# Kernel tuning notes

Hardware: AMD Instinct MI355X
Metric: run time of the kernel (lower is better)

## Reference

```python
import jax, jax.numpy as jnp
import numpy as np

N_QUBITS = 20
EVO_SUPPORT = (2, 5)
CHAIN_QUBIT = 0


def _apply_operator(state, op, support):
    """Apply batched operator op (2^k, 2^k, B) to state (2,)*n + (B,) on `support` qubits.

    Faithful to pyqtorch's apply_operator: reshape op to (2,)*2k + (B,) and contract
    the support axes, keeping the batch axis aligned.
    """
    n = state.ndim - 1
    k = len(support)
    B = state.shape[-1]
    op = op.reshape((2,) * (2 * k) + (B,))
    letters = 'abcdefghijklmnopqrstuvwxyz'
    s_l = list(letters[:n])          # state qubit axes
    b = letters[n]                   # batch axis
    out_l = list(letters[n + 1:n + 1 + k])
    in_l = [s_l[q] for q in support]
    op_str = ''.join(out_l) + ''.join(in_l) + b
    st_str = ''.join(s_l) + b
    res = list(s_l)
    for q, o in zip(support, out_l):
        res[q] = o
    return jnp.einsum(f"{op_str},{st_str}->{''.join(res) + b}", op, state)


def setup_inputs() -> dict:
    key = jax.random.key(0)
    ks = jax.random.split(key, 6)
    B = 16
    dim = 2 ** N_QUBITS
    return {
        'state_re': jax.random.normal(ks[0], (dim, B), jnp.float32),
        'state_im': jax.random.normal(ks[1], (dim, B), jnp.float32),
        'hmat_re': jax.random.normal(ks[2], (4, 4, B), jnp.float32),
        'hmat_im': jax.random.normal(ks[3], (4, 4, B), jnp.float32),
        'theta': jax.random.uniform(ks[4], (8, B), jnp.float32),
        'tvals': jax.random.uniform(ks[5], (B,), jnp.float32),
    }


def reference(state_re, state_im, hmat_re, hmat_im, theta, tvals):
    n = N_QUBITS
    B = state_re.shape[-1]
    state = (state_re + 1j * state_im).astype(jnp.complex64).reshape((2,) * n + (B,))

    # --- PyQComposedBlock: chain of single-qubit RX gates composed via reduce(bmm, reversed) ---
    half = 0.5 * theta                      # (N_ops, B)
    c = jnp.cos(half).astype(jnp.complex64)
    s = jnp.sin(half).astype(jnp.complex64)
    # U_k: [[c, -i s], [-i s, c]] per op, batch-first layout (N_ops, B, 2, 2)
    U = jnp.stack([jnp.stack([c, -1j * s], axis=-1),
                   jnp.stack([-1j * s, c], axis=-1)], axis=-2)
    acc = U[-1]
    for i in range(U.shape[0] - 2, -1, -1):  # reduce(bmm, reversed(ops)): U_{N-1} @ ... @ U_0
        acc = acc @ U[i]
    state = _apply_operator(state, jnp.moveaxis(acc, 0, -1), (CHAIN_QUBIT,))

    # --- PyQHamiltonianEvolution: U = exp(-i t H) on a 2-qubit support ---
    A = (hmat_re + 1j * hmat_im).astype(jnp.complex64)       # (4, 4, B)
    H = 0.5 * (A + jnp.conj(jnp.swapaxes(A, 0, 1)))          # Hermitian generator
    Hb = jnp.moveaxis(H, -1, 0)                              # (B, 4, 4)
    evals, V = jnp.linalg.eigh(Hb)                           # H Hermitian -> exact matrix exp
    phase = jnp.exp(-1j * tvals[:, None] * evals)            # (B, 4)
    Ue = jnp.einsum('bij,bj,bkj->bik', V, phase.astype(jnp.complex64), jnp.conj(V))
    state = _apply_operator(state, jnp.moveaxis(Ue, 0, -1), EVO_SUPPORT)

    # --- Observable: total magnetization sum_q Z_q (AddPyQOperation of diagonal Z ops) ---
    w = jnp.zeros((2,) * n, jnp.float32)
    z = jnp.array([1.0, -1.0], jnp.float32)
    for q in range(n):
        w = w + z.reshape((1,) * q + (2,) + (1,) * (n - 1 - q))
    opsi = state * w[..., None]
    # expectation Re<psi|O|psi> per batch element
    return jnp.real(jnp.sum(jnp.conj(state) * opsi, axis=tuple(range(n))))
```

## Files before the change

### kernel.cpp

```cpp
#include <hip/hip_runtime.h>
#include <math.h>

constexpr int NQ     = 20;
constexpr int DIM    = 1 << NQ;
constexpr int B      = 16;
constexpr int GROUPS = 1 << 17;
constexpr int GPB    = 32;
constexpr int TILES  = GROUPS / GPB;
constexpr int NBLK   = 1024;
constexpr int TPB    = TILES / NBLK;
constexpr int NTHR   = 512;


__global__ __launch_bounds__(256) void prep_kernel(
    const float* __restrict__ hre, const float* __restrict__ him,
    const float* __restrict__ theta, const float* __restrict__ tv,
    float* __restrict__ ws) {
  __shared__ double Mre[16][16], Mim[16][16];
  __shared__ double Are[16][16], Aim[16][16];
  __shared__ double Bre[16][16], Bim[16][16];
  __shared__ double nrm[16][4];
  __shared__ int    scl[16];
  __shared__ int    scmax_s;

  int t = threadIdx.x;
  int b = t >> 4, e = t & 15, i = e >> 2, j = e & 3;

  if (t == 0) scmax_s = 0;

  if (e == 0) {
    double th = 0.0;
    for (int k = 0; k < 8; k++) th += (double)theta[k * B + b];
    th *= 0.5;
    ws[b]     = (float)cos(th);
    ws[B + b] = (float)sin(th);
  }

  {
    double tt  = (double)tv[b];
    double are = hre[(i*4+j)*B + b], aim = him[(i*4+j)*B + b];
    double cre = hre[(j*4+i)*B + b], cim = him[(j*4+i)*B + b];
    double Hre = 0.5*(are + cre), Him = 0.5*(aim - cim);
    Mre[b][e] = tt * Him;
    Mim[b][e] = -tt * Hre;
  }
  __syncthreads();

  if (j == 0) {
    double r = 0.0;
    for (int m = 0; m < 4; m++) r += fabs(Mre[b][i*4+m]) + fabs(Mim[b][i*4+m]);
    nrm[b][i] = r;
  }
  __syncthreads();
  if (e == 0) {
    double ninf = fmax(fmax(nrm[b][0], nrm[b][1]), fmax(nrm[b][2], nrm[b][3]));
    int sc = 0;
    while (ninf > 0.25 && sc < 40) { ninf *= 0.5; sc++; }
    scl[b] = sc;
    atomicMax(&scmax_s, sc);
  }
  __syncthreads();
  int sc = scl[b];
  int scmax = scmax_s;
  {
    double scale = ldexp(1.0, -sc);
    Mre[b][e] *= scale; Mim[b][e] *= scale;
  }
  Are[b][e] = (i == j) ? 1.0 : 0.0;
  Aim[b][e] = 0.0;
  __syncthreads();

  double (*Tr)[16] = Are; double (*Ti)[16] = Aim;
  double (*Pr)[16] = Bre; double (*Pi)[16] = Bim;

  for (int k = 13; k >= 1; k--) {
    double rr = 0.0, ii = 0.0;
    for (int m = 0; m < 4; m++) {
      double mr = Mre[b][i*4+m], mi = Mim[b][i*4+m];
      double xr = Tr[b][m*4+j],  xi = Ti[b][m*4+j];
      rr += mr*xr - mi*xi;
      ii += mr*xi + mi*xr;
    }
    double inv = 1.0 / (double)k;
    Pr[b][e] = rr*inv + ((i == j) ? 1.0 : 0.0);
    Pi[b][e] = ii*inv;
    { double (*s)[16] = Tr; Tr = Pr; Pr = s; s = Ti; Ti = Pi; Pi = s; }
    __syncthreads();
  }
  for (int q = 0; q < scmax; q++) {
    double rr, ii;
    if (q < sc) {
      rr = 0.0; ii = 0.0;
      for (int m = 0; m < 4; m++) {
        double xr = Tr[b][i*4+m], xi = Ti[b][i*4+m];
        double yr = Tr[b][m*4+j], yi = Ti[b][m*4+j];
        rr += xr*yr - xi*yi;
        ii += xr*yi + xi*yr;
      }
    } else { rr = Tr[b][e]; ii = Ti[b][e]; }
    Pr[b][e] = rr; Pi[b][e] = ii;
    { double (*s)[16] = Tr; Tr = Pr; Pr = s; s = Ti; Ti = Pi; Pi = s; }
    __syncthreads();
  }

  float* ue = ws + 2*B + b*32;
  ue[e*2]     = (float)Tr[b][e];
  ue[e*2 + 1] = (float)Ti[b][e];
}

__global__ __launch_bounds__(NTHR, 6) void fused_kernel(
    const float* __restrict__ sre, const float* __restrict__ sim,
    const float* __restrict__ ws, float* __restrict__ partial) {
  __shared__ float st[16 * 512];
  __shared__ float red[16];

  int t = threadIdx.x;
  if (t < 16) red[t] = 0.f;

  int b  = t & 15;
  int gl = t >> 4;
  float c = ws[b], s = ws[B + b];
  float ur[4][4], ui[4][4];
  {
    const float* ue = ws + 2 * B + b * 32;
    #pragma unroll
    for (int i = 0; i < 4; i++) {
      float4 p0 = *(const float4*)(ue + i * 8);
      float4 p1 = *(const float4*)(ue + i * 8 + 4);
      ur[i][0] = p0.x; ui[i][0] = p0.y; ur[i][1] = p0.z; ui[i][1] = p0.w;
      ur[i][2] = p1.x; ui[i][2] = p1.y; ur[i][3] = p1.z; ui[i][3] = p1.w;
    }
  }

  int l  = t & 63;
  int wv = t >> 6;
  float acc = 0.f;

  for (int tt = 0; tt < TPB; tt++) {
    int g0 = (blockIdx.x * TPB + tt) * GPB;
    int base0 = (g0 & 0x3FFF) | ((g0 & 0xC000) << 1) | ((g0 & 0x10000) << 2);

    #pragma unroll
    for (int p = 0; p < 4; p++) {
      int cb    = p * 512 + wv * 64;
      int panel = cb >> 7;
      int wofs  = (cb & 127) << 2;
      int j     = panel >> 1;
      const float* src = (panel & 1) ? sim : sre;
      int off = (((j >> 2) & 1) << 19) | (((j >> 1) & 1) << 17) | ((j & 1) << 14);
      const float* gsrc = src + (size_t)(base0 + off) * 16 + wofs + l * 4;
      float* ldst = &st[panel * 512 + wofs];
      __builtin_amdgcn_global_load_lds(
          (const __attribute__((address_space(1))) void*)gsrc,
          (__attribute__((address_space(3))) void*)ldst,
          16, 0, 0);
    }
    __syncthreads();

    float ar[8], ai[8];
    #pragma unroll
    for (int j = 0; j < 8; j++) {
      ar[j] = st[(2 * j) * 512 + t];
      ai[j] = st[(2 * j + 1) * 512 + t];
    }

    #pragma unroll
    for (int j = 0; j < 4; j++) {
      float xr = ar[j], xi = ai[j], yr = ar[j+4], yi = ai[j+4];
      ar[j]   = c*xr + s*yi;   ai[j]   = c*xi - s*yr;
      ar[j+4] = s*xi + c*yr;   ai[j+4] = c*yi - s*xr;
    }

    int base = base0 + gl;
    int pc = __popc(base);
    float wb = (float)(17 - 2*pc);
    #pragma unroll
    for (int h = 0; h < 2; h++) {
      float w0 = wb + (h ? -1.f : 1.f);
      #pragma unroll
      for (int k = 0; k < 4; k++) {
        float rr = 0.f, ii = 0.f;
        #pragma unroll
        for (int m = 0; m < 4; m++) {
          float xr = ar[h*4+m], xi = ai[h*4+m];
          rr = fmaf(ur[k][m], xr, rr); rr = fmaf(-ui[k][m], xi, rr);
          ii = fmaf(ur[k][m], xi, ii); ii = fmaf(ui[k][m], xr, ii);
        }
        int sb = ((k>>1)&1) + (k&1);
        float w = w0 + (float)(2 - 2*sb);
        acc = fmaf(rr*rr + ii*ii, w, acc);
      }
    }
    __syncthreads();
  }

  acc += __shfl_xor(acc, 16, 64);
  acc += __shfl_xor(acc, 32, 64);

  if ((t & 63) < 16) atomicAdd(&red[t & 15], acc);
  __syncthreads();
  if (t < 16) partial[blockIdx.x * 16 + t] = red[t];
}

__global__ void reduce_kernel(const float* __restrict__ partial, float* __restrict__ out) {
  int t = threadIdx.x;
  int b = t & 15;
  float acc = 0.f;
  for (int i = t >> 4; i < NBLK; i += 16)
    acc += partial[i * 16 + b];
  acc += __shfl_xor(acc, 16, 64);
  acc += __shfl_xor(acc, 32, 64);
  __shared__ float red[16];
  if (t < 16) red[t] = 0.f;
  __syncthreads();
  if ((t & 63) < 16) atomicAdd(&red[t & 15], acc);
  __syncthreads();
  if (t < 16) out[t] = red[t];
}

extern "C" void kernel_launch(void* const* d_in, const int* in_sizes, int n_in,
                              void* d_out, int out_size, void* d_ws, size_t ws_size,
                              hipStream_t stream) {
  const float* sre = (const float*)d_in[0];
  const float* sim = (const float*)d_in[1];
  const float* hre = (const float*)d_in[2];
  const float* him = (const float*)d_in[3];
  const float* th  = (const float*)d_in[4];
  const float* tv  = (const float*)d_in[5];

  float* ws = (float*)d_ws;
  float* partial = ws + 544;

  prep_kernel<<<1, 256, 0, stream>>>(hre, him, th, tv, ws);
  fused_kernel<<<NBLK, NTHR, 0, stream>>>(sre, sim, ws, partial);
  reduce_kernel<<<1, 256, 0, stream>>>(partial, (float*)d_out);
}
```

Before: 177.7 us.

## Fuse prep, main and reduce kernels into one launch with last-block reduction

Every block now recomputes the small matrix exponential and RX rotation itself in shared memory, reusing the state-tile LDS pool, so the separate prep kernel goes away. The final reduction is done by whichever block finishes last, detected through a global atomic counter, so the separate reduce kernel also goes away. This removes two launches and their serial dependencies. In exchange each block repeats the serial double-precision prep work with many syncthreads, adds a memset, and lowers the launch-bounds occupancy hint from 6 to 2.

After: 424.4 us. +138.8%, slower.

```diff
diff --git a/kernel.cpp b/kernel.cpp
--- a/kernel.cpp
+++ b/kernel.cpp
@@ -11,124 +11,131 @@
 constexpr int TPB    = TILES / NBLK;
 constexpr int NTHR   = 512;
 
-
-__global__ __launch_bounds__(256) void prep_kernel(
+__global__ __launch_bounds__(NTHR, 2) void mega_kernel(
+    const float* __restrict__ sre, const float* __restrict__ sim,
     const float* __restrict__ hre, const float* __restrict__ him,
     const float* __restrict__ theta, const float* __restrict__ tv,
-    float* __restrict__ ws) {
-  __shared__ double Mre[16][16], Mim[16][16];
-  __shared__ double Are[16][16], Aim[16][16];
-  __shared__ double Bre[16][16], Bim[16][16];
+    float* __restrict__ partial, unsigned* __restrict__ cnt,
+    float* __restrict__ out) {
+  __shared__ double pool[4096];
+  __shared__ __align__(16) float u_f[16 * 36];
+  __shared__ float cs_lds[32];
+  __shared__ float red[16];
   __shared__ double nrm[16][4];
   __shared__ int    scl[16];
   __shared__ int    scmax_s;
+  __shared__ int    lastflag;
+
+  float*  st  = (float*)pool;
+  double* Mre = pool;
+  double* Mim = pool + 256;
+  double* Ar  = pool + 512;
+  double* Ai  = pool + 768;
+  double* Br  = pool + 1024;
+  double* Bi  = pool + 1280;
 
   int t = threadIdx.x;
-  int b = t >> 4, e = t & 15, i = e >> 2, j = e & 3;
-
-  if (t == 0) scmax_s = 0;
-
-  if (e == 0) {
-    double th = 0.0;
-    for (int k = 0; k < 8; k++) th += (double)theta[k * B + b];
-    th *= 0.5;
-    ws[b]     = (float)cos(th);
-    ws[B + b] = (float)sin(th);
-  }
+  if (t == 0) { scmax_s = 0; lastflag = 0; }
+  if (t < 16) red[t] = 0.f;
+  __syncthreads();
 
   {
-    double tt  = (double)tv[b];
-    double are = hre[(i*4+j)*B + b], aim = him[(i*4+j)*B + b];
-    double cre = hre[(j*4+i)*B + b], cim = him[(j*4+i)*B + b];
-    double Hre = 0.5*(are + cre), Him = 0.5*(aim - cim);
-    Mre[b][e] = tt * Him;
-    Mim[b][e] = -tt * Hre;
-  }
-  __syncthreads();
-
-  if (j == 0) {
-    double r = 0.0;
-    for (int m = 0; m < 4; m++) r += fabs(Mre[b][i*4+m]) + fabs(Mim[b][i*4+m]);
-    nrm[b][i] = r;
-  }
-  __syncthreads();
-  if (e == 0) {
-    double ninf = fmax(fmax(nrm[b][0], nrm[b][1]), fmax(nrm[b][2], nrm[b][3]));
-    int sc = 0;
-    while (ninf > 0.25 && sc < 40) { ninf *= 0.5; sc++; }
-    scl[b] = sc;
-    atomicMax(&scmax_s, sc);
-  }
-  __syncthreads();
-  int sc = scl[b];
-  int scmax = scmax_s;
-  {
-    double scale = ldexp(1.0, -sc);
-    Mre[b][e] *= scale; Mim[b][e] *= scale;
-  }
-  Are[b][e] = (i == j) ? 1.0 : 0.0;
-  Aim[b][e] = 0.0;
-  __syncthreads();
-
-  double (*Tr)[16] = Are; double (*Ti)[16] = Aim;
-  double (*Pr)[16] = Bre; double (*Pi)[16] = Bim;
-
-  for (int k = 13; k >= 1; k--) {
-    double rr = 0.0, ii = 0.0;
-    for (int m = 0; m < 4; m++) {
-      double mr = Mre[b][i*4+m], mi = Mim[b][i*4+m];
-      double xr = Tr[b][m*4+j],  xi = Ti[b][m*4+j];
-      rr += mr*xr - mi*xi;
-      ii += mr*xi + mi*xr;
-    }
-    double inv = 1.0 / (double)k;
-    Pr[b][e] = rr*inv + ((i == j) ? 1.0 : 0.0);
-    Pi[b][e] = ii*inv;
-    { double (*s)[16] = Tr; Tr = Pr; Pr = s; s = Ti; Ti = Pi; Pi = s; }
-    __syncthreads();
-  }
-  for (int q = 0; q < scmax; q++) {
-    double rr, ii;
-    if (q < sc) {
-      rr = 0.0; ii = 0.0;
-      for (int m = 0; m < 4; m++) {
-        double xr = Tr[b][i*4+m], xi = Ti[b][i*4+m];
-        double yr = Tr[b][m*4+j], yi = Ti[b][m*4+j];
-        rr += xr*yr - xi*yi;
-        ii += xr*yi + xi*yr;
+    int pb = (t >> 4) & 15, e = t & 15, i = e >> 2, j = e & 3;
+    bool act = (t < 256);
+
+    if (act && e == 0) {
+      double th = 0.0;
+      for (int k = 0; k < 8; k++) th += (double)theta[k * B + pb];
+      th *= 0.5;
+      cs_lds[pb]      = (float)cos(th);
+      cs_lds[16 + pb] = (float)sin(th);
+    }
+    if (act) {
+      double tt  = (double)tv[pb];
+      double are = hre[(i*4+j)*B + pb], aim = him[(i*4+j)*B + pb];
+      double cre = hre[(j*4+i)*B + pb], cim = him[(j*4+i)*B + pb];
+      double Hre = 0.5*(are + cre), Him = 0.5*(aim - cim);
+      Mre[pb*16 + e] = tt * Him;
+      Mim[pb*16 + e] = -tt * Hre;
+    }
+    __syncthreads();
+    if (act && j == 0) {
+      double r = 0.0;
+      for (int m = 0; m < 4; m++) r += fabs(Mre[pb*16 + i*4+m]) + fabs(Mim[pb*16 + i*4+m]);
+      nrm[pb][i] = r;
+    }
+    __syncthreads();
+    if (act && e == 0) {
+      double ninf = fmax(fmax(nrm[pb][0], nrm[pb][1]), fmax(nrm[pb][2], nrm[pb][3]));
+      int sc = 0;
+      while (ninf > 0.25 && sc < 40) { ninf *= 0.5; sc++; }
+      scl[pb] = sc;
+      atomicMax(&scmax_s, sc);
+    }
+    __syncthreads();
+    int scmax = scmax_s;
+    int sc = act ? scl[pb] : 0;
+    if (act) {
+      double scale = ldexp(1.0, -sc);
+      Mre[pb*16+e] *= scale; Mim[pb*16+e] *= scale;
+      Ar[pb*16+e] = (i == j) ? 1.0 : 0.0;
+      Ai[pb*16+e] = 0.0;
+    }
+    __syncthreads();
+
+    double *Tr = Ar, *Ti = Ai, *Pr = Br, *Pi = Bi;
+    for (int k = 13; k >= 1; k--) {
+      if (act) {
+        double rr = 0.0, ii = 0.0;
+        for (int m = 0; m < 4; m++) {
+          double mr = Mre[pb*16 + i*4+m], mi = Mim[pb*16 + i*4+m];
+          double xr = Tr[pb*16 + m*4+j], xi = Ti[pb*16 + m*4+j];
+          rr += mr*xr - mi*xi;
+          ii += mr*xi + mi*xr;
+        }
+        double inv = 1.0 / (double)k;
+        Pr[pb*16+e] = rr*inv + ((i == j) ? 1.0 : 0.0);
+        Pi[pb*16+e] = ii*inv;
       }
-    } else { rr = Tr[b][e]; ii = Ti[b][e]; }
-    Pr[b][e] = rr; Pi[b][e] = ii;
-    { double (*s)[16] = Tr; Tr = Pr; Pr = s; s = Ti; Ti = Pi; Pi = s; }
-    __syncthreads();
-  }
-
-  float* ue = ws + 2*B + b*32;
-  ue[e*2]     = (float)Tr[b][e];
-  ue[e*2 + 1] = (float)Ti[b][e];
-}
-
-__global__ __launch_bounds__(NTHR, 6) void fused_kernel(
-    const float* __restrict__ sre, const float* __restrict__ sim,
-    const float* __restrict__ ws, float* __restrict__ partial) {
-  __shared__ float st[16 * 512];
-  __shared__ float red[16];
-
-  int t = threadIdx.x;
-  if (t < 16) red[t] = 0.f;
-
-  int b  = t & 15;
+      { double* s0 = Tr; Tr = Pr; Pr = s0; s0 = Ti; Ti = Pi; Pi = s0; }
+      __syncthreads();
+    }
+    for (int q = 0; q < scmax; q++) {
+      if (act) {
+        double rr, ii;
+        if (q < sc) {
+          rr = 0.0; ii = 0.0;
+          for (int m = 0; m < 4; m++) {
+            double xr = Tr[pb*16 + i*4+m], xi = Ti[pb*16 + i*4+m];
+            double yr = Tr[pb*16 + m*4+j], yi = Ti[pb*16 + m*4+j];
+            rr += xr*yr - xi*yi;
+            ii += xr*yi + xi*yr;
+          }
+        } else { rr = Tr[pb*16+e]; ii = Ti[pb*16+e]; }
+        Pr[pb*16+e] = rr; Pi[pb*16+e] = ii;
+      }
+      { double* s0 = Tr; Tr = Pr; Pr = s0; s0 = Ti; Ti = Pi; Pi = s0; }
+      __syncthreads();
+    }
+    if (act) {
+      u_f[pb*36 + e*2]     = (float)Tr[pb*16+e];
+      u_f[pb*36 + e*2 + 1] = (float)Ti[pb*16+e];
+    }
+    __syncthreads();
+  }
+
+  int bb = t & 15;
   int gl = t >> 4;
-  float c = ws[b], s = ws[B + b];
+  float c = cs_lds[bb], s = cs_lds[16 + bb];
   float ur[4][4], ui[4][4];
   {
-    const float* ue = ws + 2 * B + b * 32;
-    #pragma unroll
-    for (int i = 0; i < 4; i++) {
-      float4 p0 = *(const float4*)(ue + i * 8);
-      float4 p1 = *(const float4*)(ue + i * 8 + 4);
-      ur[i][0] = p0.x; ui[i][0] = p0.y; ur[i][1] = p0.z; ui[i][1] = p0.w;
-      ur[i][2] = p1.x; ui[i][2] = p1.y; ur[i][3] = p1.z; ui[i][3] = p1.w;
+    const float* ue = u_f + bb * 36;
+    #pragma unroll
+    for (int i2 = 0; i2 < 4; i2++) {
+      float4 p0 = *(const float4*)(ue + i2 * 8);
+      float4 p1 = *(const float4*)(ue + i2 * 8 + 4);
+      ur[i2][0] = p0.x; ui[i2][0] = p0.y; ur[i2][1] = p0.z; ui[i2][1] = p0.w;
+      ur[i2][2] = p1.x; ui[i2][2] = p1.y; ur[i2][3] = p1.z; ui[i2][3] = p1.w;
     }
   }
 
@@ -136,8 +143,8 @@
   int wv = t >> 6;
   float acc = 0.f;
 
-  for (int tt = 0; tt < TPB; tt++) {
-    int g0 = (blockIdx.x * TPB + tt) * GPB;
+  for (int tt2 = 0; tt2 < TPB; tt2++) {
+    int g0 = (blockIdx.x * TPB + tt2) * GPB;
     int base0 = (g0 & 0x3FFF) | ((g0 & 0xC000) << 1) | ((g0 & 0x10000) << 2);
 
     #pragma unroll
@@ -145,9 +152,9 @@
       int cb    = p * 512 + wv * 64;
       int panel = cb >> 7;
       int wofs  = (cb & 127) << 2;
-      int j     = panel >> 1;
+      int jj    = panel >> 1;
       const float* src = (panel & 1) ? sim : sre;
-      int off = (((j >> 2) & 1) << 19) | (((j >> 1) & 1) << 17) | ((j & 1) << 14);
+      int off = (((jj >> 2) & 1) << 19) | (((jj >> 1) & 1) << 17) | ((jj & 1) << 14);
       const float* gsrc = src + (size_t)(base0 + off) * 16 + wofs + l * 4;
       float* ldst = &st[panel * 512 + wofs];
       __builtin_amdgcn_global_load_lds(
@@ -196,26 +203,29 @@
 
   acc += __shfl_xor(acc, 16, 64);
   acc += __shfl_xor(acc, 32, 64);
-
   if ((t & 63) < 16) atomicAdd(&red[t & 15], acc);
   __syncthreads();
   if (t < 16) partial[blockIdx.x * 16 + t] = red[t];
-}
-
-__global__ void reduce_kernel(const float* __restrict__ partial, float* __restrict__ out) {
-  int t = threadIdx.x;
-  int b = t & 15;
-  float acc = 0.f;
-  for (int i = t >> 4; i < NBLK; i += 16)
-    acc += partial[i * 16 + b];
-  acc += __shfl_xor(acc, 16, 64);
-  acc += __shfl_xor(acc, 32, 64);
-  __shared__ float red[16];
-  if (t < 16) red[t] = 0.f;
-  __syncthreads();
-  if ((t & 63) < 16) atomicAdd(&red[t & 15], acc);
-  __syncthreads();
-  if (t < 16) out[t] = red[t];
+  __threadfence();
+  __syncthreads();
+  if (t == 0) {
+    unsigned old = atomicAdd(cnt, 1u);
+    lastflag = (old == (unsigned)(NBLK - 1));
+  }
+  __syncthreads();
+  if (lastflag) {
+    __threadfence();
+    float a2 = 0.f;
+    for (int r = t >> 4; r < NBLK; r += 32)
+      a2 += partial[r * 16 + (t & 15)];
+    a2 += __shfl_xor(a2, 16, 64);
+    a2 += __shfl_xor(a2, 32, 64);
+    if (t < 16) red[t] = 0.f;
+    __syncthreads();
+    if ((t & 63) < 16) atomicAdd(&red[t & 15], a2);
+    __syncthreads();
+    if (t < 16) out[t] = red[t];
+  }
 }
 
 extern "C" void kernel_launch(void* const* d_in, const int* in_sizes, int n_in,
@@ -229,9 +239,10 @@
   const float* tv  = (const float*)d_in[5];
 
   float* ws = (float*)d_ws;
-  float* partial = ws + 544;
-
-  prep_kernel<<<1, 256, 0, stream>>>(hre, him, th, tv, ws);
-  fused_kernel<<<NBLK, NTHR, 0, stream>>>(sre, sim, ws, partial);
-  reduce_kernel<<<1, 256, 0, stream>>>(partial, (float*)d_out);
+  float* partial = ws;
+  unsigned* cnt = (unsigned*)((char*)d_ws + NBLK * 16 * sizeof(float));
+
+  hipMemsetAsync((void*)cnt, 0, sizeof(unsigned), stream);
+  mega_kernel<<<NBLK, NTHR, 0, stream>>>(sre, sim, hre, him, th, tv,
+                                         partial, cnt, (float*)d_out);
 }
```
